# Kernel optimization log

Hardware: AMD Instinct MI355X
Metric: run time of the kernel (lower is better)

The kernel has to match this reference:

```python
import jax, jax.numpy as jnp
import numpy as np

B, S, H = 2, 2048, 2048
NH, NKV, D = 16, 4, 128      # heads, kv heads, head_dim
GROUPS = NH // NKV
WIN = 1024                    # sliding window
EPS = 1e-5
THETA = 10000.0
NEG = -1e9


def _rms_norm(x, w):
    # over last dim (head_dim)
    var = jnp.mean(x * x, axis=-1, keepdims=True)
    return x * jax.lax.rsqrt(var + EPS) * w


def _rotate_half(x):
    x1, x2 = jnp.split(x, 2, axis=-1)
    return jnp.concatenate([-x2, x1], axis=-1)


def _apply_rope(q, k, cos, sin):
    # q: [B,NH,S,D], k: [B,NKV,S,D], cos/sin: [B,S,D]
    c = cos[:, None, :, :]
    s = sin[:, None, :, :]
    q = q * c + _rotate_half(q) * s
    k = k * c + _rotate_half(k) * s
    return q, k


def setup_inputs() -> dict:
    key = jax.random.key(0)
    ks = jax.random.split(key, 8)
    std = 0.02
    hidden_states = jax.random.normal(ks[0], (B, S, H), dtype=jnp.float32)
    Wq = jax.random.normal(ks[1], (NH * D, H), dtype=jnp.float32) * std
    Wk = jax.random.normal(ks[2], (NKV * D, H), dtype=jnp.float32) * std
    Wv = jax.random.normal(ks[3], (NKV * D, H), dtype=jnp.float32) * std
    Wo = jax.random.normal(ks[4], (H, NH * D), dtype=jnp.float32) * std
    Wg = jax.random.normal(ks[5], (NH * D, H), dtype=jnp.float32) * std
    q_norm_w = jnp.ones((D,), dtype=jnp.float32)
    k_norm_w = jnp.ones((D,), dtype=jnp.float32)
    # RoPE tables
    inv_freq = 1.0 / (THETA ** (jnp.arange(0, D, 2, dtype=jnp.float32) / D))
    pos = jnp.arange(S, dtype=jnp.float32)
    freqs = jnp.einsum('s,d->sd', pos, inv_freq)          # [S, D/2]
    emb = jnp.concatenate([freqs, freqs], axis=-1)        # [S, D]
    cos = jnp.broadcast_to(jnp.cos(emb)[None], (B, S, D)).astype(jnp.float32)
    sin = jnp.broadcast_to(jnp.sin(emb)[None], (B, S, D)).astype(jnp.float32)
    i = jnp.arange(S)[:, None]
    j = jnp.arange(S)[None, :]
    allowed = (j <= i) & (i - j < WIN)
    attention_mask = jnp.where(allowed, 0.0, NEG).astype(jnp.float32)[None, None]  # [1,1,S,S]
    return {
        'hidden_states': hidden_states, 'cos': cos, 'sin': sin,
        'attention_mask': attention_mask,
        'Wq': Wq, 'Wk': Wk, 'Wv': Wv, 'Wo': Wo, 'Wg': Wg,
        'q_norm_w': q_norm_w, 'k_norm_w': k_norm_w,
    }


def reference(hidden_states, cos, sin, attention_mask, Wq, Wk, Wv, Wo, Wg, q_norm_w, k_norm_w):
    x = hidden_states                                  # [B,S,H]
    q = (x @ Wq.T).reshape(B, S, NH, D)
    k = (x @ Wk.T).reshape(B, S, NKV, D)
    v = (x @ Wv.T).reshape(B, S, NKV, D)
    gate = x @ Wg.T                                    # [B,S,NH*D]
    q = _rms_norm(q, q_norm_w)
    k = _rms_norm(k, k_norm_w)
    q = q.transpose(0, 2, 1, 3)                        # [B,NH,S,D]
    k = k.transpose(0, 2, 1, 3)                        # [B,NKV,S,D]
    v = v.transpose(0, 2, 1, 3)
    # local (sliding) attention layer -> RoPE applied
    q, k = _apply_rope(q, k, cos, sin)
    # GQA: repeat kv heads
    k = jnp.repeat(k, GROUPS, axis=1)                  # [B,NH,S,D]
    v = jnp.repeat(v, GROUPS, axis=1)
    scaling = D ** -0.5
    scores = jnp.einsum('bhqd,bhkd->bhqk', q, k) * scaling
    scores = scores + attention_mask                   # broadcast [1,1,S,S]
    probs = jax.nn.softmax(scores.astype(jnp.float32), axis=-1).astype(q.dtype)
    out = jnp.einsum('bhqk,bhkd->bhqd', probs, v)      # [B,NH,S,D]
    out = out.transpose(0, 2, 1, 3).reshape(B, S, NH * D)
    out = out * jax.nn.sigmoid(gate)
    return out @ Wo.T                                  # [B,S,H]
```

## Files before the change

### kernel.cpp

```cpp
#include <hip/hip_runtime.h>
#include <hip/hip_bf16.h>

#define B_    2
#define S_    2048
#define H_    2048
#define NH_   16
#define NKV_  4
#define D_    128
#define WIN_  1024

typedef __attribute__((ext_vector_type(8))) short short8;
typedef __attribute__((ext_vector_type(4))) float f32x4;

__device__ __forceinline__ void gl2lds16(const void* g, void* l) {
  __builtin_amdgcn_global_load_lds(
      (const __attribute__((address_space(1))) void*)g,
      (__attribute__((address_space(3))) void*)l, 16, 0, 0);
}

__device__ __forceinline__ unsigned short f2bf(float x) {
  union { float f; unsigned int u; } v; v.f = x;
  unsigned int r = v.u + 0x7fffu + ((v.u >> 16) & 1u);
  return (unsigned short)(r >> 16);
}
__device__ __forceinline__ float bf2f(unsigned short u) {
  union { unsigned int i; float f; } v; v.i = ((unsigned int)u) << 16; return v.f;
}

#define CVT_TOTAL 5767168L
__global__ __launch_bounds__(256) void convert_all(
    const float* __restrict__ hs, const float* __restrict__ wq,
    const float* __restrict__ wk, const float* __restrict__ wv,
    const float* __restrict__ wg, const float* __restrict__ wo,
    unsigned short* __restrict__ xb, unsigned short* __restrict__ wall,
    unsigned short* __restrict__ wob) {
  long i = (long)blockIdx.x * 256 + threadIdx.x;
  if (i >= CVT_TOTAL) return;
  const float4* src; ushort4* dst;
  if (i < 2097152)      { src = (const float4*)hs + i;                         dst = (ushort4*)xb + i; }
  else if (i < 3145728) { long j = i - 2097152; src = (const float4*)wq + j;   dst = (ushort4*)wall + j; }
  else if (i < 3407872) { long j = i - 3145728; src = (const float4*)wk + j;   dst = (ushort4*)wall + 1048576 + j; }
  else if (i < 3670016) { long j = i - 3407872; src = (const float4*)wv + j;   dst = (ushort4*)wall + 1310720 + j; }
  else if (i < 4718592) { long j = i - 3670016; src = (const float4*)wg + j;   dst = (ushort4*)wall + 1572864 + j; }
  else                  { long j = i - 4718592; src = (const float4*)wo + j;   dst = (ushort4*)wob + j; }
  float4 v = *src;
  ushort4 o; o.x = f2bf(v.x); o.y = f2bf(v.y); o.z = f2bf(v.z); o.w = f2bf(v.w);
  *dst = o;
}

#define VMCNT0 asm volatile("s_waitcnt vmcnt(0)" ::: "memory")
#define VMCNT2 asm volatile("s_waitcnt vmcnt(2)" ::: "memory")
#define VMCNT3 asm volatile("s_waitcnt vmcnt(3)" ::: "memory")
#define SBAR   asm volatile("s_barrier" ::: "memory")

__global__ __launch_bounds__(512, 2) void gemm_qkvg(
    const unsigned short* __restrict__ A,
    const unsigned short* __restrict__ Bm,
    unsigned short* __restrict__ C)
{
  const int KQ = 2048, NQ = 5120;
  __shared__ unsigned short As[2][256 * 64];
  __shared__ unsigned short Bs[2][320 * 64];
  const int t = threadIdx.x;
  const int lane = t & 63;
  const int wave = t >> 6;
  const int quad = lane >> 4, rl = lane & 15;
  const int bm = blockIdx.x * 256, bn = blockIdx.y * 320;
  const int wm = (wave >> 2) * 128, wn = (wave & 3) * 80;
  const int wub = (t & ~63) * 8;

#define STAGE_A_(d, k0, rd) { int cc = (rd) * 512 + t; int row = cc >> 3;      \
    int lc = (cc & 7) ^ (row & 7);                                             \
    gl2lds16(A + (long)(bm + row) * KQ + (k0) + lc * 8,                        \
             &As[d][(rd) * 4096 + wub]); }
#define STAGE_B_(d, k0, rd) { int cc = (rd) * 512 + t; int row = cc >> 3;      \
    int lc = (cc & 7) ^ (row & 7);                                             \
    gl2lds16(Bm + (long)(bn + row) * KQ + (k0) + lc * 8,                       \
             &Bs[d][(rd) * 4096 + wub]); }
#define RD_B(c, kk) { _Pragma("unroll") for (int j = 0; j < 5; j++) {          \
    int row = wn + j * 16 + rl;                                                \
    bfr[j] = *(const short8*)(&Bs[c][row * 64 + ((((kk)*4+quad)^(row&7))*8)]); } }
#define RD_A(c, kk, f0) { _Pragma("unroll") for (int f = 0; f < 4; f++) {      \
    int row = wm + ((f0) + f) * 16 + rl;                                       \
    af[f] = *(const short8*)(&As[c][row * 64 + ((((kk)*4+quad)^(row&7))*8)]); } }
#define MM(f0) { __builtin_amdgcn_s_setprio(1);                                \
    _Pragma("unroll") for (int f = 0; f < 4; f++)                              \
    _Pragma("unroll") for (int j = 0; j < 5; j++)                              \
      acc[(f0)+f][j] = __builtin_amdgcn_mfma_f32_16x16x32_bf16(                \
          af[f], bfr[j], acc[(f0)+f][j], 0, 0, 0);                             \
    __builtin_amdgcn_s_setprio(0); }

  f32x4 acc[8][5];
#pragma unroll
  for (int f = 0; f < 8; f++)
#pragma unroll
    for (int j = 0; j < 5; j++) acc[f][j] = (f32x4){0.f, 0.f, 0.f, 0.f};

  STAGE_B_(0, 0, 0); STAGE_B_(0, 0, 1); STAGE_B_(0, 0, 2);
  STAGE_B_(0, 0, 3); STAGE_B_(0, 0, 4);
  STAGE_A_(0, 0, 0); STAGE_A_(0, 0, 2);
  STAGE_A_(0, 0, 1); STAGE_A_(0, 0, 3);
  VMCNT2; SBAR;

  for (int tk = 0; tk < 32; ++tk) {
    const int c = tk & 1, d = c ^ 1;
    const int nk0 = tk * 64 + 64;
    const bool hn = tk < 31;
    short8 af[4], bfr[5];
    RD_B(c, 0); RD_A(c, 0, 0);
    if (hn) { STAGE_B_(d, nk0, 0); STAGE_B_(d, nk0, 1); STAGE_B_(d, nk0, 2); }
    SBAR;
    MM(0);
    if (hn) { VMCNT3; } else { VMCNT0; }
    SBAR;
    RD_A(c, 0, 4);
    if (hn) { STAGE_B_(d, nk0, 3); STAGE_B_(d, nk0, 4); }
    SBAR;
    MM(4);
    SBAR;
    RD_B(c, 1); RD_A(c, 1, 0);
    if (hn) { STAGE_A_(d, nk0, 0); STAGE_A_(d, nk0, 2); }
    SBAR;
    MM(0);
    SBAR;
    RD_A(c, 1, 4);
    if (hn) { STAGE_A_(d, nk0, 1); STAGE_A_(d, nk0, 3); }
    SBAR;
    MM(4);
    if (hn) { VMCNT2; }
    SBAR;
  }

#pragma unroll
  for (int f = 0; f < 8; f++) {
    int row0 = bm + wm + f * 16 + quad * 4;
#pragma unroll
    for (int j = 0; j < 5; j++) {
      int col = bn + wn + j * 16 + rl;
#pragma unroll
      for (int r = 0; r < 4; r++)
        C[(long)(row0 + r) * NQ + col] = f2bf(acc[f][j][r]);
    }
  }
#undef STAGE_A_
#undef STAGE_B_
#undef RD_B
#undef RD_A
#undef MM
}

template <bool OUT_BF16>
__global__ __launch_bounds__(256) void gemm_bt(
    const unsigned short* __restrict__ A,
    const unsigned short* __restrict__ Bm,
    void* __restrict__ Cv, int M, int N, int K)
{
  __shared__ unsigned short Asl[128 * 64];
  __shared__ unsigned short Bsl[128 * 64];
  const int t = threadIdx.x;
  const int lane = t & 63, wave = t >> 6;
  const int quad = lane >> 4, rl = lane & 15;
  const int bm = blockIdx.x * 128, bn = blockIdx.y * 128;
  const int wm = (wave >> 1) * 64, wn = (wave & 1) * 64;
  const int ldsbase = (t & ~63) * 8;

  f32x4 acc[4][4];
#pragma unroll
  for (int i = 0; i < 4; i++)
#pragma unroll
    for (int j = 0; j < 4; j++) acc[i][j] = (f32x4){0.f, 0.f, 0.f, 0.f};

  for (int k0 = 0; k0 < K; k0 += 64) {
#pragma unroll
    for (int i = 0; i < 4; i++) {
      int tt = i * 256 + t;
      int row = tt >> 3;
      int lc = (tt & 7) ^ (row & 7);
      gl2lds16(A + (long)(bm + row) * K + k0 + lc * 8, Asl + i * 2048 + ldsbase);
      gl2lds16(Bm + (long)(bn + row) * K + k0 + lc * 8, Bsl + i * 2048 + ldsbase);
    }
    __syncthreads();
#pragma unroll
    for (int kk = 0; kk < 2; kk++) {
      short8 af[4], bfr[4];
#pragma unroll
      for (int i = 0; i < 4; i++) {
        int row = wm + i * 16 + rl;
        af[i] = *(const short8*)(Asl + row * 64 + (((kk * 4 + quad) ^ (row & 7)) * 8));
      }
#pragma unroll
      for (int j = 0; j < 4; j++) {
        int row = wn + j * 16 + rl;
        bfr[j] = *(const short8*)(Bsl + row * 64 + (((kk * 4 + quad) ^ (row & 7)) * 8));
      }
#pragma unroll
      for (int i = 0; i < 4; i++)
#pragma unroll
        for (int j = 0; j < 4; j++)
          acc[i][j] = __builtin_amdgcn_mfma_f32_16x16x32_bf16(af[i], bfr[j], acc[i][j], 0, 0, 0);
    }
    __syncthreads();
  }
#pragma unroll
  for (int i = 0; i < 4; i++) {
    int row0 = bm + wm + i * 16 + quad * 4;
#pragma unroll
    for (int j = 0; j < 4; j++) {
      int col = bn + wn + j * 16 + rl;
#pragma unroll
      for (int r = 0; r < 4; r++) {
        if (OUT_BF16)
          ((unsigned short*)Cv)[(long)(row0 + r) * N + col] = f2bf(acc[i][j][r]);
        else
          ((float*)Cv)[(long)(row0 + r) * N + col] = acc[i][j][r];
      }
    }
  }
}

__global__ __launch_bounds__(256) void pack_and_transpose(
    const unsigned short* __restrict__ qkvg,
    const float* __restrict__ cosb, const float* __restrict__ sinb,
    const float* __restrict__ qw, const float* __restrict__ kw,
    unsigned short* __restrict__ qb, unsigned short* __restrict__ kb,
    unsigned short* __restrict__ vt)
{
  __shared__ unsigned short tile[64][136];
  int t = threadIdx.x;
  if (blockIdx.x >= 20480) {
    int blk = blockIdx.x - 20480;
    int st = blk & 31, kv = (blk >> 5) & 3, b = blk >> 7;
    int s0 = st * 64;
#pragma unroll
    for (int i = 0; i < 4; i++) {
      int idx = i * 256 + t;
      int r = idx >> 4, c = (idx & 15) * 8;
      short8 v = *(const short8*)(qkvg + (long)(b * S_ + s0 + r) * 5120 + 2560 + kv * 128 + c);
      *(short8*)(&tile[r][c]) = v;
    }
    __syncthreads();
    long vo = (long)(b * NKV_ + kv) * 128;
#pragma unroll
    for (int i = 0; i < 8; i++) {
      int idx = i * 256 + t;
      int d = idx >> 4, sc = idx & 15;
      ushort4 o;
      o.x = tile[sc * 4 + 0][d]; o.y = tile[sc * 4 + 1][d];
      o.z = tile[sc * 4 + 2][d]; o.w = tile[sc * 4 + 3][d];
      *(ushort4*)(vt + (vo + d) * S_ + s0 + sc * 4) = o;
    }
    return;
  }
  int lane = t & 63, wave = t >> 6;
  long gw = (long)blockIdx.x * 4 + wave;
  int hu = (int)(gw % 20);
  long bs = gw / 20;
  int b = (int)(bs / S_);
  int s = (int)(bs % S_);
  const unsigned short* row = qkvg + bs * 5120;

  bool isq = hu < 16;
  const unsigned short* base = isq ? (row + hu * 128) : (row + 2048 + (hu - 16) * 128);
  float x1 = bf2f(base[lane]), x2 = bf2f(base[lane + 64]);
  float ss = x1 * x1 + x2 * x2;
#pragma unroll
  for (int m = 1; m < 64; m <<= 1) ss += __shfl_xor(ss, m, 64);
  float inv = rsqrtf(ss * (1.0f / 128.0f) + 1e-5f);
  const float* w = isq ? qw : kw;
  float n1 = x1 * inv * w[lane], n2 = x2 * inv * w[lane + 64];
  const float* cp = cosb + bs * 128;
  const float* sp = sinb + bs * 128;
  float o1 = n1 * cp[lane] - n2 * sp[lane];
  float o2 = n2 * cp[lane + 64] + n1 * sp[lane + 64];
  if (isq) {
    long o = ((long)(b * NH_ + hu) * S_ + s) * 128;
    qb[o + lane] = f2bf(o1); qb[o + lane + 64] = f2bf(o2);
  } else {
    long o = ((long)(b * NKV_ + (hu - 16)) * S_ + s) * 128;
    kb[o + lane] = f2bf(o1); kb[o + lane + 64] = f2bf(o2);
  }
}

#define KSTR 136
#define VSTR 72
#define PSTR 68
__global__ __launch_bounds__(256, 3) void attn_kernel(
    const unsigned short* __restrict__ qb,
    const unsigned short* __restrict__ kbuf,
    const unsigned short* __restrict__ vt,
    const unsigned short* __restrict__ qkvg,
    unsigned short* __restrict__ aout)
{
  __shared__ unsigned short Ks[64 * KSTR];
  __shared__ unsigned short Vs[128 * VSTR];
  __shared__ unsigned short Ps[4][16 * PSTR];
  int t = threadIdx.x, lane = t & 63, wave = t >> 6;
  int quad = lane >> 4, rl = lane & 15;
  int blk = blockIdx.x;
  int qt = 31 - (blk >> 5);
  int qu = blk & 3;
  int kv = (blk >> 2) & 3;
  int b  = (blk >> 4) & 1;
  int h = kv * 4 + wave;
  int q0 = qt * 64 + qu * 16;

  const unsigned short* qhead = qb + (((long)(b * NH_ + h)) * S_) * 128;
  short8 qf[4];
#pragma unroll
  for (int ks = 0; ks < 4; ks++)
    qf[ks] = *(const short8*)(qhead + (long)(q0 + rl) * 128 + ks * 32 + quad * 8);

  f32x4 oacc[8];
#pragma unroll
  for (int j = 0; j < 8; j++) oacc[j] = (f32x4){0.f, 0.f, 0.f, 0.f};
  float m_r[4], l_r[4];
#pragma unroll
  for (int r = 0; r < 4; r++) { m_r[r] = -1e9f; l_r[r] = 0.f; }

  const unsigned short* kbase_p = kbuf + ((long)(b * NKV_ + kv)) * S_ * 128;
  const unsigned short* vbase_p = vt + ((long)(b * NKV_ + kv)) * 128 * S_;
  int t_lo = qt - 16; if (t_lo < 0) t_lo = 0;

  int kr[4], kc[4], vr[4], vc[4];
#pragma unroll
  for (int i = 0; i < 4; i++) {
    int idx = i * 256 + t;
    kr[i] = idx >> 4; kc[i] = (idx & 15) * 8;
    vr[i] = idx >> 3; vc[i] = (idx & 7) * 8;
  }

  {
    int kb0 = t_lo * 64;
    short8 kv0[4], vv0[4];
#pragma unroll
    for (int i = 0; i < 4; i++) {
      kv0[i] = *(const short8*)(kbase_p + (long)(kb0 + kr[i]) * 128 + kc[i]);
      vv0[i] = *(const short8*)(vbase_p + (long)vr[i] * S_ + kb0 + vc[i]);
    }
#pragma unroll
    for (int i = 0; i < 4; i++) {
      *(short8*)(Ks + kr[i] * KSTR + kc[i]) = kv0[i];
      *(short8*)(Vs + vr[i] * VSTR + vc[i]) = vv0[i];
    }
  }
  __syncthreads();

  const float scale = 0.08838834764831845f;
  for (int kt = t_lo; kt <= qt; ++kt) {
    int kb0 = kt * 64;
    short8 kpre[4], vpre[4];
    if (kt < qt) {
      int nb0 = kb0 + 64;
#pragma unroll
      for (int i = 0; i < 4; i++) {
        kpre[i] = *(const short8*)(kbase_p + (long)(nb0 + kr[i]) * 128 + kc[i]);
        vpre[i] = *(const short8*)(vbase_p + (long)vr[i] * S_ + nb0 + vc[i]);
      }
    }

    f32x4 sc[4];
    __builtin_amdgcn_s_setprio(1);
#pragma unroll
    for (int nt = 0; nt < 4; nt++) {
      f32x4 c0 = (f32x4){0.f, 0.f, 0.f, 0.f};
#pragma unroll
      for (int ks = 0; ks < 4; ks++) {
        short8 bfrag = *(const short8*)(Ks + (nt * 16 + rl) * KSTR + (ks * 4 + quad) * 8);
        c0 = __builtin_amdgcn_mfma_f32_16x16x32_bf16(qf[ks], bfrag, c0, 0, 0, 0);
      }
      sc[nt] = c0;
    }
    __builtin_amdgcn_s_setprio(0);

#pragma unroll
    for (int nt = 0; nt < 4; nt++)
#pragma unroll
      for (int r = 0; r < 4; r++) {
        int i_row = q0 + quad * 4 + r;
        int j_col = kb0 + nt * 16 + rl;
        bool ok = (j_col <= i_row) && (i_row - j_col < WIN_);
        sc[nt][r] = ok ? sc[nt][r] * scale : -1e9f;
      }

    float mx[4];
#pragma unroll
    for (int r = 0; r < 4; r++) {
      float m0 = fmaxf(fmaxf(sc[0][r], sc[1][r]), fmaxf(sc[2][r], sc[3][r]));
#pragma unroll
      for (int m = 1; m < 16; m <<= 1) m0 = fmaxf(m0, __shfl_xor(m0, m, 64));
      mx[r] = m0;
    }
    bool need = (mx[0] > m_r[0]) | (mx[1] > m_r[1]) |
                (mx[2] > m_r[2]) | (mx[3] > m_r[3]);
    if (__any(need)) {
#pragma unroll
      for (int r = 0; r < 4; r++) {
        float newm = fmaxf(m_r[r], mx[r]);
        float alpha = __expf(m_r[r] - newm);
        l_r[r] *= alpha;
#pragma unroll
        for (int j = 0; j < 8; j++) oacc[j][r] *= alpha;
        m_r[r] = newm;
      }
    }
#pragma unroll
    for (int r = 0; r < 4; r++) {
      float p0 = __expf(sc[0][r] - m_r[r]), p1 = __expf(sc[1][r] - m_r[r]);
      float p2 = __expf(sc[2][r] - m_r[r]), p3 = __expf(sc[3][r] - m_r[r]);
      float rs = p0 + p1 + p2 + p3;
#pragma unroll
      for (int m = 1; m < 16; m <<= 1) rs += __shfl_xor(rs, m, 64);
      l_r[r] += rs;
      unsigned short* pw = &Ps[wave][(quad * 4 + r) * PSTR];
      pw[0 * 16 + rl] = f2bf(p0);
      pw[1 * 16 + rl] = f2bf(p1);
      pw[2 * 16 + rl] = f2bf(p2);
      pw[3 * 16 + rl] = f2bf(p3);
    }

    __builtin_amdgcn_s_setprio(1);
#pragma unroll
    for (int ks2 = 0; ks2 < 2; ks2++) {
      short8 af = *(const short8*)(&Ps[wave][rl * PSTR + (ks2 * 4 + quad) * 8]);
#pragma unroll
      for (int j = 0; j < 8; j++) {
        short8 bf2 = *(const short8*)(Vs + (j * 16 + rl) * VSTR + (ks2 * 4 + quad) * 8);
        oacc[j] = __builtin_amdgcn_mfma_f32_16x16x32_bf16(af, bf2, oacc[j], 0, 0, 0);
      }
    }
    __builtin_amdgcn_s_setprio(0);

    if (kt < qt) {
      __syncthreads();
#pragma unroll
      for (int i = 0; i < 4; i++) {
        *(short8*)(Ks + kr[i] * KSTR + kc[i]) = kpre[i];
        *(short8*)(Vs + vr[i] * VSTR + vc[i]) = vpre[i];
      }
      __syncthreads();
    }
  }

#pragma unroll
  for (int r = 0; r < 4; r++) {
    int s_idx = q0 + quad * 4 + r;
    float invl = 1.0f / l_r[r];
    long rowoff = (long)(b * S_ + s_idx);
    const unsigned short* gptr = qkvg + rowoff * 5120 + 3072 + h * 128;
    unsigned short* orow = aout + rowoff * 2048 + h * 128;
#pragma unroll
    for (int j = 0; j < 8; j++) {
      int d = j * 16 + rl;
      float o = oacc[j][r] * invl;
      float g = bf2f(gptr[d]);
      o = o / (1.0f + __expf(-g));
      orow[d] = f2bf(o);
    }
  }
}

extern "C" void kernel_launch(void* const* d_in, const int* in_sizes, int n_in,
                              void* d_out, int out_size, void* d_ws, size_t ws_size,
                              hipStream_t stream) {
  (void)in_sizes; (void)n_in; (void)out_size; (void)ws_size;
  const float* hs   = (const float*)d_in[0];
  const float* cosb = (const float*)d_in[1];
  const float* sinb = (const float*)d_in[2];
  const float* Wq = (const float*)d_in[4];
  const float* Wk = (const float*)d_in[5];
  const float* Wv = (const float*)d_in[6];
  const float* Wo = (const float*)d_in[7];
  const float* Wg = (const float*)d_in[8];
  const float* qw = (const float*)d_in[9];
  const float* kw = (const float*)d_in[10];
  float* out = (float*)d_out;

  char* ws = (char*)d_ws;
  unsigned short* Xb   = (unsigned short*)ws; ws += (size_t)4096 * 2048 * 2;
  unsigned short* Wall = (unsigned short*)ws; ws += (size_t)5120 * 2048 * 2;
  unsigned short* Wob  = (unsigned short*)ws; ws += (size_t)2048 * 2048 * 2;
  unsigned short* qkvg = (unsigned short*)ws; ws += (size_t)4096 * 5120 * 2;
  unsigned short* qb   = (unsigned short*)ws; ws += (size_t)B_ * NH_ * S_ * D_ * 2;
  unsigned short* kbuf = (unsigned short*)ws; ws += (size_t)B_ * NKV_ * S_ * D_ * 2;
  unsigned short* vtb  = (unsigned short*)ws; ws += (size_t)B_ * NKV_ * S_ * D_ * 2;
  unsigned short* aout = (unsigned short*)ws; ws += (size_t)4096 * 2048 * 2;

  convert_all<<<(int)((CVT_TOTAL + 255) / 256), 256, 0, stream>>>(
      hs, Wq, Wk, Wv, Wg, Wo, Xb, Wall, Wob);
  gemm_qkvg<<<dim3(16, 16), 512, 0, stream>>>(Xb, Wall, qkvg);
  pack_and_transpose<<<20736, 256, 0, stream>>>(qkvg, cosb, sinb, qw, kw, qb, kbuf, vtb);
  attn_kernel<<<1024, 256, 0, stream>>>(qb, kbuf, vtb, qkvg, aout);
  gemm_bt<false><<<dim3(32, 16), 256, 0, stream>>>(aout, Wob, (void*)out, 4096, 2048, 2048);
}
```

Baseline: 369.3 us.

## Double-buffer GEMM fragments in registers and cut per-iteration barriers

Rewrites the main K-loop of the QKV/gate projection GEMM. LDS fragments are now held in two register sets (X/Y), so later fragment reads overlap with earlier MFMA batches. The old eight barriers per iteration drop to two, and the staged global-to-LDS loads are redistributed across the phases. This trims synchronisation stalls, but it raises register pressure under the 512x2 launch bounds, which risks spills or lower occupancy.

```diff
diff --git a/kernel.cpp b/kernel.cpp
--- a/kernel.cpp
+++ b/kernel.cpp
@@ -50,7 +50,6 @@
 
 #define VMCNT0 asm volatile("s_waitcnt vmcnt(0)" ::: "memory")
 #define VMCNT2 asm volatile("s_waitcnt vmcnt(2)" ::: "memory")
-#define VMCNT3 asm volatile("s_waitcnt vmcnt(3)" ::: "memory")
 #define SBAR   asm volatile("s_barrier" ::: "memory")
 
 __global__ __launch_bounds__(512, 2) void gemm_qkvg(
@@ -77,17 +76,17 @@
     int lc = (cc & 7) ^ (row & 7);                                             \
     gl2lds16(Bm + (long)(bn + row) * KQ + (k0) + lc * 8,                       \
              &Bs[d][(rd) * 4096 + wub]); }
-#define RD_B(c, kk) { _Pragma("unroll") for (int j = 0; j < 5; j++) {          \
+#define RD_B(dst, cb, kk) { _Pragma("unroll") for (int j = 0; j < 5; j++) {    \
     int row = wn + j * 16 + rl;                                                \
-    bfr[j] = *(const short8*)(&Bs[c][row * 64 + ((((kk)*4+quad)^(row&7))*8)]); } }
-#define RD_A(c, kk, f0) { _Pragma("unroll") for (int f = 0; f < 4; f++) {      \
+    dst[j] = *(const short8*)(&Bs[cb][row * 64 + ((((kk)*4+quad)^(row&7))*8)]); } }
+#define RD_A(dst, cb, kk, f0) { _Pragma("unroll") for (int f = 0; f < 4; f++) {\
     int row = wm + ((f0) + f) * 16 + rl;                                       \
-    af[f] = *(const short8*)(&As[c][row * 64 + ((((kk)*4+quad)^(row&7))*8)]); } }
-#define MM(f0) { __builtin_amdgcn_s_setprio(1);                                \
+    dst[f] = *(const short8*)(&As[cb][row * 64 + ((((kk)*4+quad)^(row&7))*8)]); } }
+#define MM(a_, b_, f0) { __builtin_amdgcn_s_setprio(1);                        \
     _Pragma("unroll") for (int f = 0; f < 4; f++)                              \
     _Pragma("unroll") for (int j = 0; j < 5; j++)                              \
       acc[(f0)+f][j] = __builtin_amdgcn_mfma_f32_16x16x32_bf16(                \
-          af[f], bfr[j], acc[(f0)+f][j], 0, 0, 0);                             \
+          a_[f], b_[j], acc[(f0)+f][j], 0, 0, 0);                              \
     __builtin_amdgcn_s_setprio(0); }
 
   f32x4 acc[8][5];
@@ -100,35 +99,27 @@
   STAGE_B_(0, 0, 3); STAGE_B_(0, 0, 4);
   STAGE_A_(0, 0, 0); STAGE_A_(0, 0, 2);
   STAGE_A_(0, 0, 1); STAGE_A_(0, 0, 3);
-  VMCNT2; SBAR;
+  VMCNT0; SBAR;
+
+  short8 afX[4], bfrX[5], afY[4], bfrY[5];
 
   for (int tk = 0; tk < 32; ++tk) {
     const int c = tk & 1, d = c ^ 1;
     const int nk0 = tk * 64 + 64;
     const bool hn = tk < 31;
-    short8 af[4], bfr[5];
-    RD_B(c, 0); RD_A(c, 0, 0);
+    RD_B(bfrX, c, 0); RD_A(afX, c, 0, 0);
+    VMCNT0; SBAR;
+    RD_A(afY, c, 0, 4);
     if (hn) { STAGE_B_(d, nk0, 0); STAGE_B_(d, nk0, 1); STAGE_B_(d, nk0, 2); }
-    SBAR;
-    MM(0);
-    if (hn) { VMCNT3; } else { VMCNT0; }
-    SBAR;
-    RD_A(c, 0, 4);
-    if (hn) { STAGE_B_(d, nk0, 3); STAGE_B_(d, nk0, 4); }
-    SBAR;
-    MM(4);
-    SBAR;
-    RD_B(c, 1); RD_A(c, 1, 0);
-    if (hn) { STAGE_A_(d, nk0, 0); STAGE_A_(d, nk0, 2); }
-    SBAR;
-    MM(0);
-    SBAR;
-    RD_A(c, 1, 4);
-    if (hn) { STAGE_A_(d, nk0, 1); STAGE_A_(d, nk0, 3); }
-    SBAR;
-    MM(4);
-    if (hn) { VMCNT2; }
-    SBAR;
+    MM(afX, bfrX, 0);
+    RD_B(bfrY, c, 1); RD_A(afX, c, 1, 0);
+    if (hn) { STAGE_B_(d, nk0, 3); STAGE_B_(d, nk0, 4); STAGE_A_(d, nk0, 0); }
+    MM(afY, bfrX, 4);
+    RD_A(afY, c, 1, 4);
+    if (hn) { STAGE_A_(d, nk0, 2); STAGE_A_(d, nk0, 1); STAGE_A_(d, nk0, 3); }
+    MM(afX, bfrY, 0);
+    MM(afY, bfrY, 4);
+    VMCNT2; SBAR;
   }
 
 #pragma unroll
```

Result: slower. 386.3 us (+4.6%).
